# Performance work log

Hardware: AMD Instinct MI355X
Metric: run time of the kernel (lower is better)

The kernel has to match this reference:

```python
import jax, jax.numpy as jnp
import numpy as np

B, S, M_DIM, N_DIM, K_NNZ = 8, 2048, 2048, 2048, 205


def setup_inputs() -> dict:
    key = jax.random.key(0)
    k1, k2, k3, k4 = jax.random.split(key, 4)
    x = jax.random.normal(k1, (B, S, M_DIM), dtype=jnp.float32)
    # CSR structure: K_NNZ unique, sorted column indices per row
    scores = jax.random.uniform(k2, (N_DIM, M_DIM))
    cols = jnp.sort(jnp.argsort(scores, axis=1)[:, :K_NNZ], axis=1)  # [N, K] unique per row
    indices = cols.reshape(-1).astype(jnp.int32)                      # [nnz]
    indptr = (jnp.arange(N_DIM + 1) * K_NNZ).astype(jnp.int32)        # [N+1]
    W_val = jax.random.normal(k3, (N_DIM * K_NNZ,), dtype=jnp.float32) * (1.0 / np.sqrt(M_DIM))
    bias = jax.random.normal(k4, (N_DIM,), dtype=jnp.float32) * 0.01
    return {"x": x, "W_val": W_val, "bias": bias, "indices": indices, "indptr": indptr}


def reference(x, W_val, bias, indices, indptr):
    # SparseLinear.forward: y = x @ W^T + bias, with W stored in CSR
    # (W_val: nnz values, indptr: [N+1] row pointers, indices: [nnz] column ids).
    N = indptr.shape[0] - 1
    M = x.shape[-1]
    nnz = W_val.shape[0]
    # row id of each nonzero, derived from indptr (standard CSR expansion)
    row_ids = jnp.searchsorted(indptr, jnp.arange(nnz, dtype=indptr.dtype), side="right") - 1
    # materialize the sparse weight (CSR columns are unique per row -> set is exact)
    W = jnp.zeros((N, M), dtype=W_val.dtype).at[row_ids, indices].set(W_val)
    return jnp.einsum("bsm,nm->bsn", x, W) + bias
```

## Files before the change

kernel.cpp:

```cpp
#include <hip/hip_runtime.h>
#include <hip/hip_bf16.h>
#include <stdint.h>

#define M_TOT 16384
#define K_TOT 2048
#define N_TOT 2048

#define BM 256
#define BN 256
#define BK 64
#define LDS_HALF (128 * 64)

typedef __attribute__((ext_vector_type(8))) short short8;
typedef __attribute__((ext_vector_type(4))) float float4v;
typedef __attribute__((ext_vector_type(8))) unsigned short ushort8;
typedef __attribute__((ext_vector_type(4))) unsigned short ushort4v;

__device__ __forceinline__ unsigned short f2bf_rne(float f) {
    union { float f; unsigned u; } a; a.f = f;
    unsigned r = a.u + 0x7FFFu + ((a.u >> 16) & 1u);
    return (unsigned short)(r >> 16);
}

__global__ __launch_bounds__(256) void densify_kernel(
    const float* __restrict__ val, const int* __restrict__ idx,
    const int* __restrict__ indptr, unsigned short* __restrict__ Wb) {
    const int n = blockIdx.x;
    unsigned short* row = Wb + (size_t)n * K_TOT;
    ushort8 z = {0, 0, 0, 0, 0, 0, 0, 0};
    ((ushort8*)row)[threadIdx.x] = z;
    __syncthreads();
    const int s = indptr[n], e = indptr[n + 1];
    for (int j = s + (int)threadIdx.x; j < e; j += (int)blockDim.x)
        row[idx[j]] = f2bf_rne(val[j]);
}

#define CAST_GRID 2048
__global__ __launch_bounds__(256) void cast_kernel(
    const float* __restrict__ x, unsigned short* __restrict__ xb) {
    const float4* xf = (const float4*)x;
    size_t i = (size_t)blockIdx.x * 256 + threadIdx.x;
    const size_t stride = (size_t)CAST_GRID * 256;
#pragma unroll
    for (int it = 0; it < 16; ++it, i += stride) {
        float4 a = xf[i];
        ushort4v o;
        o[0] = f2bf_rne(a.x); o[1] = f2bf_rne(a.y);
        o[2] = f2bf_rne(a.z); o[3] = f2bf_rne(a.w);
        ((ushort4v*)xb)[i] = o;
    }
}

__global__ __launch_bounds__(512, 2) void gemm_bias_kernel_256(
    const unsigned short* __restrict__ A,
    const unsigned short* __restrict__ Bw,
    const float* __restrict__ bias,
    float* __restrict__ C)
{
    extern __shared__ unsigned short lds[];

    const int tid  = threadIdx.x;
    const int lane = tid & 63;
    const int wave = tid >> 6;

    const int raw = blockIdx.x;
    const int lid = (raw & 7) * 64 + (raw >> 3);
    const int bm = lid >> 3;
    const int bn = lid & 7;

    const int wrow = wave >> 2;
    const int wcol = wave & 3;
    const int wr16 = wrow * 16;
    const int wc16 = wcol * 16;
    const int mrow = lane & 15;
    const int quad = lane >> 4;
    const int rx   = mrow & 7;

    const int srow = lane >> 3;
    const int csrc = ((lane & 7) ^ srow) * 8;
    const unsigned short* pA = A  + (size_t)(bm * BM + wave * 8 + srow) * K_TOT + csrc;
    const unsigned short* pB = Bw + (size_t)(bn * BN + wave * 8 + srow) * K_TOT + csrc;
    unsigned short* lw = lds + wave * 8 * 64;

    float4v acc[8][4] = {};
    short8 af[4][2];
    short8 bfr[2][2];

#define STAGE(PG, MATIDX, BUF, H, K0)                                            \
    { _Pragma("unroll")                                                          \
      for (int l = 0; l < 2; ++l) {                                              \
        const unsigned short* g = (PG) + ((size_t)((H) * 128 + l * 64) * K_TOT + (size_t)(K0)); \
        unsigned short* lp = lw + (((BUF) * 4 + (MATIDX) * 2 + (H)) * LDS_HALF) + l * 64 * 64;  \
        __builtin_amdgcn_global_load_lds(                                        \
            (const __attribute__((address_space(1))) unsigned int*)g,            \
            (__attribute__((address_space(3))) unsigned int*)lp, 16, 0, 0);      \
      } }

#define WAITV4 asm volatile("s_waitcnt vmcnt(4)" ::: "memory")
#define WAITV0 asm volatile("s_waitcnt vmcnt(0)" ::: "memory")
#define NOSTG  ((void)0)
#define NOWT   ((void)0)

#define PHASE(BUF, MH, NH, DOA, DOB, STG, TAILW)                                 \
  {                                                                              \
    if (DOA) {                                                                   \
      const unsigned short* Ah = lds + ((BUF) * 4 + (MH)) * LDS_HALF;            \
      _Pragma("unroll")                                                          \
      for (int mi = 0; mi < 4; ++mi) {                                           \
        const int r = mi * 32 + wr16 + mrow;                                     \
        _Pragma("unroll")                                                        \
        for (int ks = 0; ks < 2; ++ks)                                           \
          af[mi][ks] = *(const short8*)(Ah + r * 64 + (((ks * 4 + quad) ^ rx) * 8)); \
      }                                                                          \
    }                                                                            \
    if (DOB) {                                                                   \
      const unsigned short* Bh = lds + ((BUF) * 4 + 2 + (NH)) * LDS_HALF;        \
      _Pragma("unroll")                                                          \
      for (int ni = 0; ni < 2; ++ni) {                                           \
        const int r = ni * 64 + wc16 + mrow;                                     \
        _Pragma("unroll")                                                        \
        for (int ks = 0; ks < 2; ++ks)                                           \
          bfr[ni][ks] = *(const short8*)(Bh + r * 64 + (((ks * 4 + quad) ^ rx) * 8)); \
      }                                                                          \
    }                                                                            \
    STG;                                                                         \
    asm volatile("" ::: "memory");                                               \
    __builtin_amdgcn_s_barrier();                                                \
    asm volatile("s_waitcnt lgkmcnt(0)" ::: "memory");                           \
    __builtin_amdgcn_s_setprio(1);                                               \
    _Pragma("unroll")                                                            \
    for (int mi = 0; mi < 4; ++mi)                                               \
      _Pragma("unroll")                                                          \
      for (int ni = 0; ni < 2; ++ni)                                             \
        _Pragma("unroll")                                                        \
        for (int ks = 0; ks < 2; ++ks)                                           \
          acc[(MH) * 4 + mi][(NH) * 2 + ni] =                                    \
              __builtin_amdgcn_mfma_f32_16x16x32_bf16(                           \
                  af[mi][ks], bfr[ni][ks], acc[(MH) * 4 + mi][(NH) * 2 + ni], 0, 0, 0); \
    __builtin_amdgcn_s_setprio(0);                                               \
    TAILW;                                                                       \
    asm volatile("" ::: "memory");                                               \
    __builtin_amdgcn_s_barrier();                                                \
    asm volatile("" ::: "memory");                                               \
  }

    STAGE(pA, 0, 0, 0, 0);
    STAGE(pB, 1, 0, 1, 0);
    STAGE(pB, 1, 0, 0, 0);
    STAGE(pA, 0, 0, 1, 0);
    STAGE(pA, 0, 1, 0, 64);
    STAGE(pB, 1, 1, 1, 64);
    WAITV4;
    asm volatile("" ::: "memory");
    __builtin_amdgcn_s_barrier();
    asm volatile("" ::: "memory");

    int k0b = 64, k0c = 128, k0d = 192;
#pragma unroll 1
    for (int it = 0; it < 15; ++it) {
        PHASE(0, 0, 0, 1, 1, STAGE(pB, 1, 1, 0, k0b), NOWT)
        PHASE(0, 0, 1, 0, 1, STAGE(pA, 0, 1, 1, k0b), NOWT)
        PHASE(0, 1, 1, 1, 0, STAGE(pA, 0, 0, 0, k0c), NOWT)
        PHASE(0, 1, 0, 0, 1, STAGE(pB, 1, 0, 1, k0c), WAITV4)
        PHASE(1, 0, 0, 1, 1, STAGE(pB, 1, 0, 0, k0c), NOWT)
        PHASE(1, 0, 1, 0, 1, STAGE(pA, 0, 0, 1, k0c), NOWT)
        PHASE(1, 1, 1, 1, 0, STAGE(pA, 0, 1, 0, k0d), NOWT)
        PHASE(1, 1, 0, 0, 1, STAGE(pB, 1, 1, 1, k0d), WAITV4)
        k0b += 128; k0c += 128; k0d += 128;
    }
    PHASE(0, 0, 0, 1, 1, STAGE(pB, 1, 1, 0, k0b), NOWT)
    PHASE(0, 0, 1, 0, 1, STAGE(pA, 0, 1, 1, k0b), NOWT)
    PHASE(0, 1, 1, 1, 0, NOSTG, NOWT)
    PHASE(0, 1, 0, 0, 1, NOSTG, WAITV0)
    PHASE(1, 0, 0, 1, 1, NOSTG, NOWT)
    PHASE(1, 0, 1, 0, 1, NOSTG, NOWT)
    PHASE(1, 1, 1, 1, 0, NOSTG, NOWT)
    PHASE(1, 1, 0, 0, 1, NOSTG, NOWT)

#pragma unroll
    for (int nh = 0; nh < 2; ++nh)
#pragma unroll
        for (int ni = 0; ni < 2; ++ni) {
            const int col = bn * BN + nh * 128 + ni * 64 + wc16 + mrow;
            const float bv = bias[col];
#pragma unroll
            for (int mh = 0; mh < 2; ++mh)
#pragma unroll
                for (int mi = 0; mi < 4; ++mi) {
                    const int row0 = bm * BM + mh * 128 + mi * 32 + wr16 + quad * 4;
#pragma unroll
                    for (int r = 0; r < 4; ++r)
                        C[(size_t)(row0 + r) * N_TOT + col] =
                            acc[mh * 4 + mi][nh * 2 + ni][r] + bv;
                }
        }
#undef PHASE
#undef STAGE
#undef WAITV4
#undef WAITV0
#undef NOSTG
#undef NOWT
}

#define FBM 128
#define FBN 128
#define FBK 64
__global__ __launch_bounds__(256) void gemm_bias_kernel_128(
    const unsigned short* __restrict__ A,
    const unsigned short* __restrict__ Bw,
    const float* __restrict__ bias,
    float* __restrict__ C)
{
    __shared__ unsigned short Asm[FBM * FBK];
    __shared__ unsigned short Bsm[FBN * FBK];

    const int tid  = threadIdx.x;
    const int lane = tid & 63;
    const int wave = tid >> 6;
    const int bm = blockIdx.y;
    const int bn = blockIdx.x;

    const int srow_l = lane >> 3;
    const int schunk = ((lane & 7) ^ srow_l) * 8;
    const unsigned short* a_g[4];
    const unsigned short* b_g[4];
    unsigned short* a_l[4];
    unsigned short* b_l[4];
#pragma unroll
    for (int l = 0; l < 4; ++l) {
        const int row = wave * 32 + l * 8 + srow_l;
        a_g[l] = A  + (size_t)(bm * FBM + row) * K_TOT + schunk;
        b_g[l] = Bw + (size_t)(bn * FBN + row) * K_TOT + schunk;
        a_l[l] = Asm + (wave * 32 + l * 8) * FBK;
        b_l[l] = Bsm + (wave * 32 + l * 8) * FBK;
    }

    const int wm = (wave >> 1) * 64;
    const int wn = (wave & 1) * 64;
    const int mrow = lane & 15;
    const int quad = lane >> 4;
    const int rx   = mrow & 7;

    float4v acc[4][4] = {};

    for (int k0 = 0; k0 < K_TOT; k0 += FBK) {
        __syncthreads();
#pragma unroll
        for (int l = 0; l < 4; ++l)
            __builtin_amdgcn_global_load_lds(
                (const __attribute__((address_space(1))) unsigned int*)(a_g[l] + k0),
                (__attribute__((address_space(3))) unsigned int*)a_l[l], 16, 0, 0);
#pragma unroll
        for (int l = 0; l < 4; ++l)
            __builtin_amdgcn_global_load_lds(
                (const __attribute__((address_space(1))) unsigned int*)(b_g[l] + k0),
                (__attribute__((address_space(3))) unsigned int*)b_l[l], 16, 0, 0);
        __syncthreads();

#pragma unroll
        for (int ks = 0; ks < 2; ++ks) {
            short8 af[4], bf_[4];
#pragma unroll
            for (int mi = 0; mi < 4; ++mi) {
                const int r = wm + mi * 16 + mrow;
                const int slot = (ks * 4 + quad) ^ rx;
                af[mi] = *(const short8*)(Asm + r * FBK + slot * 8);
            }
#pragma unroll
            for (int ni = 0; ni < 4; ++ni) {
                const int r = wn + ni * 16 + mrow;
                const int slot = (ks * 4 + quad) ^ rx;
                bf_[ni] = *(const short8*)(Bsm + r * FBK + slot * 8);
            }
#pragma unroll
            for (int mi = 0; mi < 4; ++mi)
#pragma unroll
                for (int ni = 0; ni < 4; ++ni)
                    acc[mi][ni] = __builtin_amdgcn_mfma_f32_16x16x32_bf16(
                        af[mi], bf_[ni], acc[mi][ni], 0, 0, 0);
        }
    }

#pragma unroll
    for (int ni = 0; ni < 4; ++ni) {
        const int col = bn * FBN + wn + ni * 16 + mrow;
        const float bv = bias[col];
#pragma unroll
        for (int mi = 0; mi < 4; ++mi) {
#pragma unroll
            for (int r = 0; r < 4; ++r) {
                const int row = bm * FBM + wm + mi * 16 + quad * 4 + r;
                C[(size_t)row * N_TOT + col] = acc[mi][ni][r] + bv;
            }
        }
    }
}

extern "C" void kernel_launch(void* const* d_in, const int* in_sizes, int n_in,
                              void* d_out, int out_size, void* d_ws, size_t ws_size,
                              hipStream_t stream) {
    const float* x       = (const float*)d_in[0];
    const float* W_val   = (const float*)d_in[1];
    const float* bias    = (const float*)d_in[2];
    const int*   indices = (const int*)d_in[3];
    const int*   indptr  = (const int*)d_in[4];
    float* out = (float*)d_out;

    unsigned short* xb = (unsigned short*)d_ws;
    unsigned short* Wb = xb + (size_t)M_TOT * K_TOT;
    if (ws_size < ((size_t)M_TOT * K_TOT + (size_t)N_TOT * K_TOT) * sizeof(unsigned short))
        return;

    hipError_t attr_ok = hipFuncSetAttribute(
        reinterpret_cast<const void*>(gemm_bias_kernel_256),
        hipFuncAttributeMaxDynamicSharedMemorySize, 131072);

    cast_kernel<<<CAST_GRID, 256, 0, stream>>>(x, xb);
    densify_kernel<<<N_TOT, 256, 0, stream>>>(W_val, indices, indptr, Wb);

    if (attr_ok == hipSuccess) {
        gemm_bias_kernel_256<<<dim3(512), 512, 131072, stream>>>(xb, Wb, bias, out);
    } else {
        dim3 grid(N_TOT / FBN, M_TOT / FBM);
        gemm_bias_kernel_128<<<grid, 256, 0, stream>>>(xb, Wb, bias, out);
    }
}
```

Before: 348.0 us.

## Prefetch next phase LDS fragments after MFMAs and cut per-phase barriers

Restructures the 8-phase GEMM pipeline so LDS fragment reads for the next phase are issued at the end of the current phase, after its MFMAs and global-to-LDS staging. The B fragments are double-buffered by N-half so they can stay live across phases. Each phase now has one barrier instead of two. The goal is to hide LDS read latency behind MFMA work and reduce synchronisation overhead, at the cost of more registers and riskier ordering between LDS reads and async overwrites.

```diff
diff --git a/kernel.cpp b/kernel.cpp
--- a/kernel.cpp
+++ b/kernel.cpp
@@ -84,7 +84,7 @@
 
     float4v acc[8][4] = {};
     short8 af[4][2];
-    short8 bfr[2][2];
+    short8 bfr[2][2][2];
 
 #define STAGE(PG, MATIDX, BUF, H, K0)                                            \
     { _Pragma("unroll")                                                          \
@@ -96,36 +96,39 @@
             (__attribute__((address_space(3))) unsigned int*)lp, 16, 0, 0);      \
       } }
 
-#define WAITV4 asm volatile("s_waitcnt vmcnt(4)" ::: "memory")
-#define WAITV0 asm volatile("s_waitcnt vmcnt(0)" ::: "memory")
-#define NOSTG  ((void)0)
-#define NOWT   ((void)0)
-
-#define PHASE(BUF, MH, NH, DOA, DOB, STG, TAILW)                                 \
-  {                                                                              \
-    if (DOA) {                                                                   \
-      const unsigned short* Ah = lds + ((BUF) * 4 + (MH)) * LDS_HALF;            \
+#define RD_A(RBUF, RMH)                                                          \
+    { const unsigned short* Ah = lds + ((RBUF) * 4 + (RMH)) * LDS_HALF;          \
       _Pragma("unroll")                                                          \
       for (int mi = 0; mi < 4; ++mi) {                                           \
         const int r = mi * 32 + wr16 + mrow;                                     \
         _Pragma("unroll")                                                        \
         for (int ks = 0; ks < 2; ++ks)                                           \
           af[mi][ks] = *(const short8*)(Ah + r * 64 + (((ks * 4 + quad) ^ rx) * 8)); \
-      }                                                                          \
-    }                                                                            \
-    if (DOB) {                                                                   \
-      const unsigned short* Bh = lds + ((BUF) * 4 + 2 + (NH)) * LDS_HALF;        \
+      } }
+
+#define RD_B(RBUF, RNH)                                                          \
+    { const unsigned short* Bh = lds + ((RBUF) * 4 + 2 + (RNH)) * LDS_HALF;      \
       _Pragma("unroll")                                                          \
       for (int ni = 0; ni < 2; ++ni) {                                           \
         const int r = ni * 64 + wc16 + mrow;                                     \
         _Pragma("unroll")                                                        \
         for (int ks = 0; ks < 2; ++ks)                                           \
-          bfr[ni][ks] = *(const short8*)(Bh + r * 64 + (((ks * 4 + quad) ^ rx) * 8)); \
-      }                                                                          \
-    }                                                                            \
-    STG;                                                                         \
-    asm volatile("" ::: "memory");                                               \
-    __builtin_amdgcn_s_barrier();                                                \
+          bfr[RNH][ni][ks] = *(const short8*)(Bh + r * 64 + (((ks * 4 + quad) ^ rx) * 8)); \
+      } }
+
+#define BARX { asm volatile("" ::: "memory"); __builtin_amdgcn_s_barrier(); asm volatile("" ::: "memory"); }
+#define NOB  ((void)0);
+#define WAITV4 asm volatile("s_waitcnt vmcnt(4)" ::: "memory")
+#define WAITV0 asm volatile("s_waitcnt vmcnt(0)" ::: "memory")
+#define WV4B { WAITV4; BARX }
+#define WV0B { WAITV0; BARX }
+#define NOWT ((void)0)
+#define NOSTG ((void)0)
+#define NORD ((void)0)
+
+#define PHASE(MH, NH, BHEAD, STG, TAILW, RDS)                                    \
+  {                                                                              \
+    BHEAD                                                                        \
     asm volatile("s_waitcnt lgkmcnt(0)" ::: "memory");                           \
     __builtin_amdgcn_s_setprio(1);                                               \
     _Pragma("unroll")                                                            \
@@ -136,12 +139,11 @@
         for (int ks = 0; ks < 2; ++ks)                                           \
           acc[(MH) * 4 + mi][(NH) * 2 + ni] =                                    \
               __builtin_amdgcn_mfma_f32_16x16x32_bf16(                           \
-                  af[mi][ks], bfr[ni][ks], acc[(MH) * 4 + mi][(NH) * 2 + ni], 0, 0, 0); \
+                  af[mi][ks], bfr[NH][ni][ks], acc[(MH) * 4 + mi][(NH) * 2 + ni], 0, 0, 0); \
     __builtin_amdgcn_s_setprio(0);                                               \
+    STG;                                                                         \
     TAILW;                                                                       \
-    asm volatile("" ::: "memory");                                               \
-    __builtin_amdgcn_s_barrier();                                                \
-    asm volatile("" ::: "memory");                                               \
+    RDS;                                                                         \
   }
 
     STAGE(pA, 0, 0, 0, 0);
@@ -151,31 +153,30 @@
     STAGE(pA, 0, 1, 0, 64);
     STAGE(pB, 1, 1, 1, 64);
     WAITV4;
-    asm volatile("" ::: "memory");
-    __builtin_amdgcn_s_barrier();
-    asm volatile("" ::: "memory");
+    BARX
+    RD_A(0, 0); RD_B(0, 0);
 
     int k0b = 64, k0c = 128, k0d = 192;
 #pragma unroll 1
     for (int it = 0; it < 15; ++it) {
-        PHASE(0, 0, 0, 1, 1, STAGE(pB, 1, 1, 0, k0b), NOWT)
-        PHASE(0, 0, 1, 0, 1, STAGE(pA, 0, 1, 1, k0b), NOWT)
-        PHASE(0, 1, 1, 1, 0, STAGE(pA, 0, 0, 0, k0c), NOWT)
-        PHASE(0, 1, 0, 0, 1, STAGE(pB, 1, 0, 1, k0c), WAITV4)
-        PHASE(1, 0, 0, 1, 1, STAGE(pB, 1, 0, 0, k0c), NOWT)
-        PHASE(1, 0, 1, 0, 1, STAGE(pA, 0, 0, 1, k0c), NOWT)
-        PHASE(1, 1, 1, 1, 0, STAGE(pA, 0, 1, 0, k0d), NOWT)
-        PHASE(1, 1, 0, 0, 1, STAGE(pB, 1, 1, 1, k0d), WAITV4)
+        PHASE(0, 0, NOB,  STAGE(pB, 1, 1, 0, k0b), NOWT, RD_B(0, 1))
+        PHASE(0, 1, BARX, STAGE(pA, 0, 1, 1, k0b), NOWT, RD_A(0, 1))
+        PHASE(1, 1, BARX, STAGE(pA, 0, 0, 0, k0c), NOWT, NORD)
+        PHASE(1, 0, BARX, STAGE(pB, 1, 0, 1, k0c), WV4B, RD_A(1, 0); RD_B(1, 0))
+        PHASE(0, 0, NOB,  STAGE(pB, 1, 0, 0, k0c), NOWT, RD_B(1, 1))
+        PHASE(0, 1, BARX, STAGE(pA, 0, 0, 1, k0c), NOWT, RD_A(1, 1))
+        PHASE(1, 1, BARX, STAGE(pA, 0, 1, 0, k0d), NOWT, NORD)
+        PHASE(1, 0, BARX, STAGE(pB, 1, 1, 1, k0d), WV4B, RD_A(0, 0); RD_B(0, 0))
         k0b += 128; k0c += 128; k0d += 128;
     }
-    PHASE(0, 0, 0, 1, 1, STAGE(pB, 1, 1, 0, k0b), NOWT)
-    PHASE(0, 0, 1, 0, 1, STAGE(pA, 0, 1, 1, k0b), NOWT)
-    PHASE(0, 1, 1, 1, 0, NOSTG, NOWT)
-    PHASE(0, 1, 0, 0, 1, NOSTG, WAITV0)
-    PHASE(1, 0, 0, 1, 1, NOSTG, NOWT)
-    PHASE(1, 0, 1, 0, 1, NOSTG, NOWT)
-    PHASE(1, 1, 1, 1, 0, NOSTG, NOWT)
-    PHASE(1, 1, 0, 0, 1, NOSTG, NOWT)
+    PHASE(0, 0, NOB,  STAGE(pB, 1, 1, 0, k0b), NOWT, RD_B(0, 1))
+    PHASE(0, 1, BARX, STAGE(pA, 0, 1, 1, k0b), NOWT, RD_A(0, 1))
+    PHASE(1, 1, BARX, NOSTG, NOWT, NORD)
+    PHASE(1, 0, BARX, NOSTG, WV0B, RD_A(1, 0); RD_B(1, 0))
+    PHASE(0, 0, NOB,  NOSTG, NOWT, RD_B(1, 1))
+    PHASE(0, 1, BARX, NOSTG, NOWT, RD_A(1, 1))
+    PHASE(1, 1, BARX, NOSTG, NOWT, NORD)
+    PHASE(1, 0, BARX, NOSTG, NOWT, NORD)
 
 #pragma unroll
     for (int nh = 0; nh < 2; ++nh)
@@ -196,10 +197,17 @@
         }
 #undef PHASE
 #undef STAGE
+#undef RD_A
+#undef RD_B
+#undef BARX
+#undef NOB
 #undef WAITV4
 #undef WAITV0
+#undef WV4B
+#undef WV0B
+#undef NOWT
 #undef NOSTG
-#undef NOWT
+#undef NORD
 }
 
 #define FBM 128
```

Result: no change. 346.8 us (-0.3%).
